# Kernel optimization log

Measured on AMD Instinct MI355X. Metric: run time of the kernel, lower is better.

The kernel has to match this reference:

```python
import jax, jax.numpy as jnp
import numpy as np
from jax import lax

HEADS, DIM_HEAD, KSZ = 8, 64, 3


def conv1x1(x, w):
    # x: [B, Cin, X, Y], w: [Cout, Cin]
    return jnp.einsum('oi,bixy->boxy', w, x)


def setup_inputs() -> dict:
    key = jax.random.key(0)
    ks = jax.random.split(key, 8)
    dim = 256
    inner = HEADS * DIM_HEAD  # 512
    B, H, W = 4, 64, 64
    s = 0.02
    return {
        'fmap': jax.random.normal(ks[0], (B, dim, H, W), jnp.float32),
        'w_lin_q': jax.random.normal(ks[1], (inner, dim), jnp.float32) * s,
        'w_lin_kv_dw': jax.random.normal(ks[2], (dim, 1, 3, 3), jnp.float32) * s,
        'w_lin_kv_pw': jax.random.normal(ks[3], (2 * inner, dim), jnp.float32) * s,
        'w_q': jax.random.normal(ks[4], (inner, dim), jnp.float32) * s,
        'w_kv': jax.random.normal(ks[5], (2 * inner, dim), jnp.float32) * s,
        'w_out': jax.random.normal(ks[6], (dim, 2 * inner), jnp.float32) * s,
        'b_out': jax.random.normal(ks[7], (dim,), jnp.float32) * s,
    }


def reference(fmap, w_lin_q, w_lin_kv_dw, w_lin_kv_pw, w_q, w_kv, w_out, b_out):
    B, dim, X, Y = fmap.shape
    h, d, ksz = HEADS, DIM_HEAD, KSZ
    scale = d ** -0.5
    n = X * Y

    # ---- linear (global) attention branch ----
    # depthwise 3x3 conv (groups=dim) then pointwise 1x1, both bias-free
    dw = lax.conv_general_dilated(
        fmap, w_lin_kv_dw, window_strides=(1, 1), padding=[(1, 1), (1, 1)],
        dimension_numbers=('NCHW', 'OIHW', 'NCHW'), feature_group_count=dim)
    lin_kv = conv1x1(dw, w_lin_kv_pw)
    lin_q = conv1x1(fmap, w_lin_q)
    lin_k, lin_v = jnp.split(lin_kv, 2, axis=1)

    def to_bhnd(t):  # [B, h*d, X, Y] -> [B, h, n, d]
        return t.reshape(B, h, d, n).transpose(0, 1, 3, 2)

    lq, lk, lv = to_bhnd(lin_q), to_bhnd(lin_k), to_bhnd(lin_v)
    lq = jax.nn.softmax(lq, axis=-1) * scale   # softmax over feature dim
    lk = jax.nn.softmax(lk, axis=-2)           # softmax over sequence dim
    ctx = jnp.einsum('bhnd,bhne->bhde', lk, lv)
    lin_out = jnp.einsum('bhnd,bhde->bhne', lq, ctx)
    lin_out = lin_out.transpose(0, 1, 3, 2).reshape(B, h * d, X, Y)
    lin_out = jax.nn.gelu(lin_out, approximate=False)  # torch nn.GELU (exact erf)

    # ---- local window attention branch (unfold equivalent) ----
    q = conv1x1(fmap, w_q).reshape(B, h, d, X, Y) * scale
    kv = conv1x1(fmap, w_kv)
    k, v = jnp.split(kv, 2, axis=1)
    k = k.reshape(B, h, d, X, Y)
    v = v.reshape(B, h, d, X, Y)
    pad = ksz // 2
    padw = ((0, 0), (0, 0), (0, 0), (pad, pad), (pad, pad))
    kp = jnp.pad(k, padw)  # zero padding, as in F.unfold
    vp = jnp.pad(v, padw)
    # j enumerates kernel offsets row-major (ky, kx) -> matches F.unfold layout
    k_win = jnp.stack([kp[..., i:i + X, j:j + Y]
                       for i in range(ksz) for j in range(ksz)], axis=2)  # [B,h,j,d,X,Y]
    v_win = jnp.stack([vp[..., i:i + X, j:j + Y]
                       for i in range(ksz) for j in range(ksz)], axis=2)
    sim = jnp.einsum('bhdxy,bhjdxy->bhxyj', q, k_win)
    attn = jax.nn.softmax(sim, axis=-1)  # stable (max-subtracted internally)
    full = jnp.einsum('bhxyj,bhjdxy->bhdxy', attn, v_win)
    full = full.reshape(B, h * d, X, Y)

    out = jnp.concatenate([lin_out, full], axis=1)  # [B, 2*inner, X, Y]
    return conv1x1(out, w_out) + b_out[None, :, None, None]
```

## Files before the change

kernel.cpp:

```cpp
#include <hip/hip_runtime.h>
#include <cmath>

#define NPIX 4096
#define NTOT 16384
#define CIN  256

typedef __bf16 bf16x8 __attribute__((ext_vector_type(8)));
typedef float  f32x4  __attribute__((ext_vector_type(4)));
typedef unsigned short u16x8 __attribute__((ext_vector_type(8)));

static __device__ __forceinline__ unsigned short f2bf(float f) {
    unsigned u = __float_as_uint(f);
    unsigned r = (u + 0x7FFFu + ((u >> 16) & 1u)) >> 16;
    return (unsigned short)r;
}
static __device__ __forceinline__ float bf2f(unsigned short u) {
    return __uint_as_float((unsigned)u << 16);
}

__global__ __launch_bounds__(256) void k_transpose_bf(const float* __restrict__ src,
                                                      unsigned short* __restrict__ dst) {
    __shared__ float tile[64][65];
    int p0 = blockIdx.x * 64;
    int c0 = blockIdx.y * 64;
    int b  = blockIdx.z;
    int t = threadIdx.x;
    int tp = t & 63, tg = t >> 6;
    const float* s = src + ((size_t)(b * 256 + c0) * 4096) + p0;
#pragma unroll
    for (int r = 0; r < 16; ++r) {
        int c = r * 4 + tg;
        tile[tp][c] = s[(size_t)c * 4096 + tp];
    }
    __syncthreads();
    unsigned short* d = dst + ((size_t)(b * 4096 + p0)) * 256 + c0;
#pragma unroll
    for (int r = 0; r < 16; ++r) {
        int pr = r * 4 + tg;
        d[(size_t)pr * 256 + tp] = f2bf(tile[pr][tp]);
    }
}

__global__ __launch_bounds__(256) void k_dwconv_bf(const unsigned short* __restrict__ FMB,
                                                   const float* __restrict__ wdw,
                                                   unsigned short* __restrict__ DWB) {
    __shared__ float wl[2560];
    int t = threadIdx.x;
    for (int i = t; i < 2304; i += 256) wl[(i / 9) * 10 + (i % 9)] = wdw[i];
    __syncthreads();
    int idx = blockIdx.x * 256 + t;
    int cg = idx & 31, p = idx >> 5;
    int xy = p & 4095, x = xy >> 6, y = xy & 63;
    const unsigned short* base = FMB + (size_t)p * 256 + cg * 8;
    float s[8] = {0.f, 0.f, 0.f, 0.f, 0.f, 0.f, 0.f, 0.f};
#pragma unroll
    for (int dx = 0; dx < 3; ++dx) {
        int xx = x + dx - 1;
        if ((unsigned)xx >= 64u) continue;
#pragma unroll
        for (int dy = 0; dy < 3; ++dy) {
            int yy = y + dy - 1;
            if ((unsigned)yy >= 64u) continue;
            u16x8 v = *(const u16x8*)(base + ((dx - 1) * 64 + (dy - 1)) * 256);
#pragma unroll
            for (int d = 0; d < 8; ++d)
                s[d] += bf2f(v[d]) * wl[(cg * 8 + d) * 10 + dx * 3 + dy];
        }
    }
    uint4 w0;
    w0.x = (unsigned)f2bf(s[0]) | ((unsigned)f2bf(s[1]) << 16);
    w0.y = (unsigned)f2bf(s[2]) | ((unsigned)f2bf(s[3]) << 16);
    w0.z = (unsigned)f2bf(s[4]) | ((unsigned)f2bf(s[5]) << 16);
    w0.w = (unsigned)f2bf(s[6]) | ((unsigned)f2bf(s[7]) << 16);
    *(uint4*)(DWB + (size_t)p * 256 + cg * 8) = w0;
}

__global__ __launch_bounds__(256) void k_convert_w(const float* __restrict__ w1, const float* __restrict__ w2,
                                                   const float* __restrict__ w3, const float* __restrict__ w4,
                                                   const float* __restrict__ w5,
                                                   unsigned short* __restrict__ dst) {
    int i = blockIdx.x * 256 + threadIdx.x;
    float v;
    if (i < 131072)       v = w1[i];
    else if (i < 262144)  v = w2[i - 131072];
    else if (i < 524288)  v = w3[i - 262144];
    else if (i < 786432) {
        int elem = i - 524288;
        int rp = elem >> 8, c = elem & 255;
        int h = rp >> 7, wi = rp & 127;
        int srow = (wi < 64) ? (h * 64 + wi) : (512 + h * 64 + (wi - 64));
        v = w4[srow * 256 + c];
    } else                v = w5[i - 786432];
    dst[i] = f2bf(v);
}

__global__ __launch_bounds__(256) void k_g1_gemm(const __bf16* __restrict__ A,
                                                 const __bf16* __restrict__ B,
                                                 unsigned short* __restrict__ LQBT,
                                                 unsigned short* __restrict__ CKV2T) {
    __shared__ __align__(16) __bf16 SMEM[32768];
    const int K = 256;
    const int m0 = blockIdx.x * 128;
    const int n0 = blockIdx.y * 128;
    const int t = threadIdx.x;
    const int w = t >> 6, l = t & 63;
    const int wm = (w >> 1) * 64, wn = (w & 1) * 64;
    f32x4 acc[4][4];
#pragma unroll
    for (int i = 0; i < 4; ++i)
#pragma unroll
        for (int j = 0; j < 4; ++j) acc[i][j] = (f32x4){0.f, 0.f, 0.f, 0.f};

    const int lrow = l >> 3;
    const int lchunk = (l & 7) ^ lrow;
    auto STAGE = [&](int buf, int k0) {
#pragma unroll
        for (int r = 0; r < 4; ++r) {
            const int s = w + r * 4;
            const int row = s * 8 + lrow;
            const __bf16* ga = A + (size_t)(m0 + row) * K + (k0 + lchunk * 8);
            const __bf16* gb = B + (size_t)(n0 + row) * K + (k0 + lchunk * 8);
            __builtin_amdgcn_global_load_lds((const __attribute__((address_space(1))) void*)ga,
                                             (__attribute__((address_space(3))) void*)(SMEM + buf * 16384 + s * 512),
                                             16, 0, 0);
            __builtin_amdgcn_global_load_lds((const __attribute__((address_space(1))) void*)gb,
                                             (__attribute__((address_space(3))) void*)(SMEM + buf * 16384 + 8192 + s * 512),
                                             16, 0, 0);
        }
    };
    STAGE(0, 0);
    STAGE(1, 64);
#pragma unroll
    for (int it = 0; it < 4; ++it) {
        if (it < 3) { asm volatile("s_waitcnt vmcnt(8)" ::: "memory"); }
        else        { asm volatile("s_waitcnt vmcnt(0)" ::: "memory"); }
        __builtin_amdgcn_sched_barrier(0);
        __builtin_amdgcn_s_barrier();
        __builtin_amdgcn_sched_barrier(0);
        const __bf16* As = SMEM + (it & 1) * 16384;
        const __bf16* Bs = As + 8192;
#pragma unroll
        for (int ks = 0; ks < 2; ++ks) {
            bf16x8 af[4], bfr[4];
#pragma unroll
            for (int i = 0; i < 4; ++i) {
                const int arow = wm + i * 16 + (l & 15);
                const int ac = ((l >> 4) + ks * 4) ^ (l & 7);
                af[i] = *(const bf16x8*)(As + arow * 64 + ac * 8);
                const int brow = wn + i * 16 + (l & 15);
                bfr[i] = *(const bf16x8*)(Bs + brow * 64 + ac * 8);
            }
#pragma unroll
            for (int i = 0; i < 4; ++i)
#pragma unroll
                for (int j = 0; j < 4; ++j)
                    acc[i][j] = __builtin_amdgcn_mfma_f32_16x16x32_bf16(af[i], bfr[j], acc[i][j], 0, 0, 0);
        }
        __builtin_amdgcn_sched_barrier(0);
        __builtin_amdgcn_s_barrier();
        __builtin_amdgcn_sched_barrier(0);
        if (it < 2) STAGE(it & 1, (it + 2) * 64);
    }

#pragma unroll
    for (int i = 0; i < 4; ++i) {
        const int prow = wm + i * 16 + (l >> 4) * 4;
#pragma unroll
        for (int j = 0; j < 4; ++j) {
            const int col = wn + j * 16 + (l & 15);
            const int cglob = n0 + col;
            const float sc = (cglob >= 512 && cglob < 1024) ? 0.125f : 1.f;
#pragma unroll
            for (int q = 0; q < 4; ++q)
                *((unsigned short*)SMEM + (prow + q) * 136 + col) = f2bf(acc[i][j][q] * sc);
        }
    }
    __syncthreads();
    const int pix = t >> 1, half = t & 1;
    unsigned short* sp = (unsigned short*)SMEM + pix * 136 + half * 64;
    if (n0 < 512) {
        float m = -1e30f;
#pragma unroll
        for (int r = 0; r < 8; ++r) {
            u16x8 v = *(const u16x8*)(sp + r * 8);
#pragma unroll
            for (int d = 0; d < 8; ++d) m = fmaxf(m, bf2f(v[d]));
        }
        float Z = 0.f;
#pragma unroll
        for (int r = 0; r < 8; ++r) {
            u16x8 v = *(const u16x8*)(sp + r * 8);
            u16x8 e;
#pragma unroll
            for (int d = 0; d < 8; ++d) {
                float ev = __expf(bf2f(v[d]) - m);
                Z += ev;
                e[d] = f2bf(ev);
            }
            *(u16x8*)(sp + r * 8) = e;
        }
        float inv = 0.125f / Z;
        unsigned short* dst = LQBT + ((size_t)(n0 >> 7) << 21) + (size_t)m0 * 128 + t * 64;
#pragma unroll
        for (int r = 0; r < 8; ++r) {
            u16x8 e = *(const u16x8*)(sp + r * 8);
            float o[8];
#pragma unroll
            for (int d = 0; d < 8; ++d) o[d] = bf2f(e[d]) * inv;
            uint4 wv;
            wv.x = (unsigned)f2bf(o[0]) | ((unsigned)f2bf(o[1]) << 16);
            wv.y = (unsigned)f2bf(o[2]) | ((unsigned)f2bf(o[3]) << 16);
            wv.z = (unsigned)f2bf(o[4]) | ((unsigned)f2bf(o[5]) << 16);
            wv.w = (unsigned)f2bf(o[6]) | ((unsigned)f2bf(o[7]) << 16);
            *(uint4*)(dst + r * 8) = wv;
        }
    } else {
        unsigned short* dptr = CKV2T + ((size_t)((n0 - 512) >> 7) << 21) + (size_t)m0 * 128 + t * 64;
#pragma unroll
        for (int r = 0; r < 8; ++r)
            *(u16x8*)(dptr + r * 8) = *(const u16x8*)(sp + r * 8);
    }
}

__global__ __launch_bounds__(256) void k_g2_gemm(const __bf16* __restrict__ A,
                                                 const __bf16* __restrict__ B,
                                                 float* __restrict__ PART,
                                                 float* __restrict__ S) {
    __shared__ __align__(16) __bf16 SMEM[32768];
    const int K = 256;
    const int m0 = blockIdx.x * 128;
    const int n0 = blockIdx.y * 128;
    const int t = threadIdx.x;
    const int w = t >> 6, l = t & 63;
    const int wm = (w >> 1) * 64, wn = (w & 1) * 64;
    f32x4 acc[4][4];
#pragma unroll
    for (int i = 0; i < 4; ++i)
#pragma unroll
        for (int j = 0; j < 4; ++j) acc[i][j] = (f32x4){0.f, 0.f, 0.f, 0.f};

    const int lrow = l >> 3;
    const int lchunk = (l & 7) ^ lrow;
    auto STAGE = [&](int buf, int k0) {
#pragma unroll
        for (int r = 0; r < 4; ++r) {
            const int s = w + r * 4;
            const int row = s * 8 + lrow;
            const __bf16* ga = A + (size_t)(m0 + row) * K + (k0 + lchunk * 8);
            const __bf16* gb = B + (size_t)(n0 + row) * K + (k0 + lchunk * 8);
            __builtin_amdgcn_global_load_lds((const __attribute__((address_space(1))) void*)ga,
                                             (__attribute__((address_space(3))) void*)(SMEM + buf * 16384 + s * 512),
                                             16, 0, 0);
            __builtin_amdgcn_global_load_lds((const __attribute__((address_space(1))) void*)gb,
                                             (__attribute__((address_space(3))) void*)(SMEM + buf * 16384 + 8192 + s * 512),
                                             16, 0, 0);
        }
    };
    STAGE(0, 0);
    STAGE(1, 64);
#pragma unroll
    for (int it = 0; it < 4; ++it) {
        if (it < 3) { asm volatile("s_waitcnt vmcnt(8)" ::: "memory"); }
        else        { asm volatile("s_waitcnt vmcnt(0)" ::: "memory"); }
        __builtin_amdgcn_sched_barrier(0);
        __builtin_amdgcn_s_barrier();
        __builtin_amdgcn_sched_barrier(0);
        const __bf16* As = SMEM + (it & 1) * 16384;
        const __bf16* Bs = As + 8192;
#pragma unroll
        for (int ks = 0; ks < 2; ++ks) {
            bf16x8 af[4], bfr[4];
#pragma unroll
            for (int i = 0; i < 4; ++i) {
                const int arow = wm + i * 16 + (l & 15);
                const int ac = ((l >> 4) + ks * 4) ^ (l & 7);
                af[i] = *(const bf16x8*)(As + arow * 64 + ac * 8);
                const int brow = wn + i * 16 + (l & 15);
                bfr[i] = *(const bf16x8*)(Bs + brow * 64 + ac * 8);
            }
#pragma unroll
            for (int i = 0; i < 4; ++i)
#pragma unroll
                for (int j = 0; j < 4; ++j)
                    acc[i][j] = __builtin_amdgcn_mfma_f32_16x16x32_bf16(af[i], bfr[j], acc[i][j], 0, 0, 0);
        }
        __builtin_amdgcn_sched_barrier(0);
        __builtin_amdgcn_s_barrier();
        __builtin_amdgcn_sched_barrier(0);
        if (it < 2) STAGE(it & 1, (it + 2) * 64);
    }

    unsigned short* ST = (unsigned short*)SMEM;
#pragma unroll
    for (int i = 0; i < 4; ++i) {
        const int prow = wm + i * 16 + (l >> 4) * 4;
#pragma unroll
        for (int j = 0; j < 4; ++j) {
            const int col = wn + j * 16 + (l & 15);
#pragma unroll
            for (int q = 0; q < 4; ++q) {
                float v = acc[i][j][q];
                ST[col * 130 + prow + q] = f2bf(col < 64 ? __expf(v) : v);
            }
        }
    }
    __syncthreads();
    const int h  = blockIdx.y;
    const int bh = (m0 >> 12) * 8 + h;
    const int dm = (w >> 1) * 32, en = (w & 1) * 32;
    f32x4 c2[2][2];
    f32x4 s2[2];
#pragma unroll
    for (int i = 0; i < 2; ++i) {
        s2[i] = (f32x4){0.f, 0.f, 0.f, 0.f};
#pragma unroll
        for (int j = 0; j < 2; ++j) c2[i][j] = (f32x4){0.f, 0.f, 0.f, 0.f};
    }
    bf16x8 ones;
#pragma unroll
    for (int d = 0; d < 8; ++d) ones[d] = (__bf16)1.0f;
#pragma unroll
    for (int kp = 0; kp < 4; ++kp) {
        bf16x8 af2[2], bv2[2];
#pragma unroll
        for (int i = 0; i < 2; ++i) {
            const int drow = dm + i * 16 + (l & 15);
            af2[i] = *(const bf16x8*)(ST + drow * 130 + kp * 32 + (l >> 4) * 8);
            const int erow = 64 + en + i * 16 + (l & 15);
            bv2[i] = *(const bf16x8*)(ST + erow * 130 + kp * 32 + (l >> 4) * 8);
        }
#pragma unroll
        for (int i = 0; i < 2; ++i)
#pragma unroll
            for (int j = 0; j < 2; ++j)
                c2[i][j] = __builtin_amdgcn_mfma_f32_16x16x32_bf16(af2[i], bv2[j], c2[i][j], 0, 0, 0);
        if ((w & 1) == 0)
#pragma unroll
            for (int i = 0; i < 2; ++i)
                s2[i] = __builtin_amdgcn_mfma_f32_16x16x32_bf16(af2[i], ones, s2[i], 0, 0, 0);
    }
    float* pp = PART + ((size_t)((m0 >> 7) * 8 + h)) * 4096 + t * 16;
#pragma unroll
    for (int i = 0; i < 2; ++i)
#pragma unroll
        for (int j = 0; j < 2; ++j)
            *(f32x4*)(pp + (i * 2 + j) * 4) = c2[i][j];
    if ((w & 1) == 0 && (l & 15) == 0) {
#pragma unroll
        for (int i = 0; i < 2; ++i)
#pragma unroll
            for (int q = 0; q < 4; ++q)
                atomicAdd(&S[bh * 64 + dm + i * 16 + (l >> 4) * 4 + q], s2[i][q]);
    }
}

__global__ __launch_bounds__(256) void k_ctxnorm(const float* __restrict__ PART,
                                                 const float* __restrict__ S,
                                                 unsigned short* __restrict__ ctxb) {
    __shared__ float SUM[1024];
    __shared__ float sinv[32];
    const int bh = blockIdx.x, wq = blockIdx.y;
    const int b = bh >> 3, h = bh & 7;
    const int t = threadIdx.x;
    const int bd = (wq >> 1) * 32, be = (wq & 1) * 32;
#pragma unroll
    for (int r = 0; r < 4; ++r) {
        const int kl = t + 256 * r;
        const float* src = PART + (size_t)((b * 32) * 8 + h) * 4096 + wq * 1024 + kl;
        float s = 0.f;
#pragma unroll
        for (int mi = 0; mi < 32; ++mi)
            s += src[(size_t)mi * 8 * 4096];
        SUM[kl] = s;
    }
    if (t < 32) sinv[t] = 1.f / S[bh * 64 + bd + t];
    __syncthreads();
#pragma unroll
    for (int r = 0; r < 4; ++r) {
        const int idx = t + 256 * r;
        const int dd = idx & 31, ee = idx >> 5;
        const int d = bd + dd, e = be + ee;
        const int l2 = (((d >> 2) & 3) << 4) | (e & 15);
        const int i2 = (d >> 4) & 1, j2 = (e >> 4) & 1, q = d & 3;
        const int kl = l2 * 16 + (i2 * 2 + j2) * 4 + q;
        ctxb[(size_t)bh * 4096 + e * 64 + d] = f2bf(SUM[kl] * sinv[dd]);
    }
}

__global__ __launch_bounds__(256) void k_out_gemm(const __bf16* __restrict__ A,
                                                  const __bf16* __restrict__ B,
                                                  float* __restrict__ C,
                                                  const float* __restrict__ bias) {
    __shared__ __align__(16) __bf16 SMEM[24576];
    const int K = 1024;
    const int m0 = blockIdx.x * 64, n0 = blockIdx.y * 128;
    const int t = threadIdx.x;
    const int w = t >> 6, l = t & 63;
    const int wm = (w >> 1) * 32, wn = (w & 1) * 64;
    f32x4 acc[2][4];
#pragma unroll
    for (int i = 0; i < 2; ++i)
#pragma unroll
        for (int j = 0; j < 4; ++j) acc[i][j] = (f32x4){0.f, 0.f, 0.f, 0.f};

    const int lrow = l >> 3;
    const int lchunk = (l & 7) ^ lrow;
    auto STAGE = [&](int buf, int k0) {
        __bf16* As = SMEM + buf * 12288;
        __bf16* Bs = As + 4096;
#pragma unroll
        for (int r = 0; r < 2; ++r) {
            const int s = w + r * 4;
            const int row = s * 8 + lrow;
            const __bf16* ga = A + (size_t)(m0 + row) * K + (k0 + lchunk * 8);
            __builtin_amdgcn_global_load_lds((const __attribute__((address_space(1))) void*)ga,
                                             (__attribute__((address_space(3))) void*)(As + s * 512),
                                             16, 0, 0);
        }
#pragma unroll
        for (int r = 0; r < 4; ++r) {
            const int s = w + r * 4;
            const int row = s * 8 + lrow;
            const __bf16* gb = B + (size_t)(n0 + row) * K + (k0 + lchunk * 8);
            __builtin_amdgcn_global_load_lds((const __attribute__((address_space(1))) void*)gb,
                                             (__attribute__((address_space(3))) void*)(Bs + s * 512),
                                             16, 0, 0);
        }
    };

    STAGE(0, 0);
    STAGE(1, 64);
    for (int it = 0; it < 16; ++it) {
        if (it < 15) { asm volatile("s_waitcnt vmcnt(6)" ::: "memory"); }
        else         { asm volatile("s_waitcnt vmcnt(0)" ::: "memory"); }
        __builtin_amdgcn_sched_barrier(0);
        __builtin_amdgcn_s_barrier();
        __builtin_amdgcn_sched_barrier(0);
        const __bf16* As = SMEM + (it & 1) * 12288;
        const __bf16* Bs = As + 4096;
#pragma unroll
        for (int ks = 0; ks < 2; ++ks) {
            const int ac = ((l >> 4) + ks * 4) ^ (l & 7);
            bf16x8 af[2], bfr[4];
#pragma unroll
            for (int i = 0; i < 2; ++i) {
                const int arow = wm + i * 16 + (l & 15);
                af[i] = *(const bf16x8*)(As + arow * 64 + ac * 8);
            }
#pragma unroll
            for (int j = 0; j < 4; ++j) {
                const int brow = wn + j * 16 + (l & 15);
                bfr[j] = *(const bf16x8*)(Bs + brow * 64 + ac * 8);
            }
#pragma unroll
            for (int i = 0; i < 2; ++i)
#pragma unroll
                for (int j = 0; j < 4; ++j)
                    acc[i][j] = __builtin_amdgcn_mfma_f32_16x16x32_bf16(af[i], bfr[j], acc[i][j], 0, 0, 0);
        }
        __builtin_amdgcn_sched_barrier(0);
        __builtin_amdgcn_s_barrier();
        __builtin_amdgcn_sched_barrier(0);
        if (it < 14) STAGE(it & 1, (it + 2) * 64);
    }
    const int b = m0 >> 12;
#pragma unroll
    for (int j = 0; j < 4; ++j) {
        const int col = n0 + wn + j * 16 + (l & 15);
        const float bv = bias[col];
        float* obase = C + ((size_t)(b * 256 + col) << 12);
#pragma unroll
        for (int i = 0; i < 2; ++i) {
            const int rb = (m0 & 4095) + wm + i * 16 + (l >> 4) * 4;
            f32x4 v = acc[i][j];
            v[0] += bv; v[1] += bv; v[2] += bv; v[3] += bv;
            *(f32x4*)(obase + rb) = v;
        }
    }
}

__global__ __launch_bounds__(256) void k_linlocal(const __bf16* __restrict__ LQBT,
                                                  const __bf16* __restrict__ ctxb,
                                                  const unsigned short* __restrict__ CKV,
                                                  unsigned short* __restrict__ CAT) {
    const int bid = blockIdx.x;
    const int t = threadIdx.x;
    if (bid < 1024) {
        const int p0 = (bid & 127) * 128;
        const int h  = bid >> 7;
        const int b  = p0 >> 12;
        const int w = t >> 6, l = t & 63;
        const int wm = w * 32;
        const __bf16* Bm = ctxb + (size_t)(b * 8 + h) * 4096;
        const __bf16* Ah = LQBT + ((size_t)(h >> 1) << 21) + (h & 1) * 64;
        f32x4 acc[2][4];
#pragma unroll
        for (int i = 0; i < 2; ++i)
#pragma unroll
            for (int j = 0; j < 4; ++j) acc[i][j] = (f32x4){0.f, 0.f, 0.f, 0.f};
#pragma unroll
        for (int ks = 0; ks < 2; ++ks) {
            const int c = (l >> 4) + ks * 4;
            bf16x8 af[2], bfr[4];
#pragma unroll
            for (int i = 0; i < 2; ++i) {
                const int row = p0 + wm + i * 16 + (l & 15);
                af[i] = *(const bf16x8*)(Ah + (size_t)row * 128 + c * 8);
            }
#pragma unroll
            for (int j = 0; j < 4; ++j) {
                const int erow = j * 16 + (l & 15);
                bfr[j] = *(const bf16x8*)(Bm + erow * 64 + c * 8);
            }
#pragma unroll
            for (int i = 0; i < 2; ++i)
#pragma unroll
                for (int j = 0; j < 4; ++j)
                    acc[i][j] = __builtin_amdgcn_mfma_f32_16x16x32_bf16(af[i], bfr[j], acc[i][j], 0, 0, 0);
        }
#pragma unroll
        for (int i = 0; i < 2; ++i) {
#pragma unroll
            for (int j = 0; j < 4; ++j) {
                const int e = j * 16 + (l & 15);
#pragma unroll
                for (int q = 0; q < 4; ++q) {
                    const int p = p0 + wm + i * 16 + (l >> 4) * 4 + q;
                    float x = acc[i][j][q];
                    float g = 0.5f * x * (1.f + erff(x * 0.70710678118654752f));
                    CAT[(size_t)p * 1024 + h * 64 + e] = f2bf(g);
                }
            }
        }
    } else {
        const int W = (bid - 1024) * 4 + (t >> 6);
        const int lane = t & 63;
        const int h = W & 7;
        const int G = W >> 3;
        const int yg = G & 7, x = (G >> 3) & 63, b = G >> 9;
        const int lg = lane >> 3, c8 = lane & 7;
        const int y = (yg << 3) + lg;
        const int p = (b << 12) + (x << 6) + y;
        const unsigned short* Qp = CKV + ((size_t)(h >> 1) << 21) + (size_t)p * 128 + (h & 1) * 64 + c8 * 8;
        const unsigned short* Kp = Qp + ((size_t)4 << 21);
        const unsigned short* Vp = Qp + ((size_t)8 << 21);

        const bool okx[3] = {x > 0, true, x < 63};
        const bool oky[3] = {y > 0, true, y < 63};
        bool okn[9]; int ofs[9];
#pragma unroll
        for (int dx = 0; dx < 3; ++dx)
#pragma unroll
            for (int dy = 0; dy < 3; ++dy) {
                const int k = dx * 3 + dy;
                okn[k] = okx[dx] && oky[dy];
                ofs[k] = okn[k] ? ((dx - 1) * 64 + (dy - 1)) * 128 : 0;
            }
        float qf[8];
        {
            u16x8 q8 = *(const u16x8*)Qp;
#pragma unroll
            for (int d = 0; d < 8; ++d) qf[d] = bf2f(q8[d]);
        }
        float sim[9];
#pragma unroll
        for (int k = 0; k < 9; ++k) {
            u16x8 k8 = *(const u16x8*)(Kp + ofs[k]);
            float s = 0.f;
#pragma unroll
            for (int d = 0; d < 8; ++d) s += qf[d] * bf2f(k8[d]);
            s = okn[k] ? s : 0.f;
            s += __shfl_xor(s, 1);
            s += __shfl_xor(s, 2);
            s += __shfl_xor(s, 4);
            sim[k] = s;
        }
        float mx = sim[0];
#pragma unroll
        for (int k = 1; k < 9; ++k) mx = fmaxf(mx, sim[k]);
        float a[9], Z = 0.f;
#pragma unroll
        for (int k = 0; k < 9; ++k) { a[k] = __expf(sim[k] - mx); Z += a[k]; }
        float inv = 1.f / Z;
#pragma unroll
        for (int k = 0; k < 9; ++k) a[k] = okn[k] ? a[k] * inv : 0.f;
        float o[8] = {0.f, 0.f, 0.f, 0.f, 0.f, 0.f, 0.f, 0.f};
#pragma unroll
        for (int k = 0; k < 9; ++k) {
            u16x8 v8 = *(const u16x8*)(Vp + ofs[k]);
#pragma unroll
            for (int d = 0; d < 8; ++d) o[d] += a[k] * bf2f(v8[d]);
        }
        unsigned short* dst = CAT + (size_t)p * 1024 + 512 + h * 64 + c8 * 8;
        uint4 w0;
        w0.x = (unsigned)f2bf(o[0]) | ((unsigned)f2bf(o[1]) << 16);
        w0.y = (unsigned)f2bf(o[2]) | ((unsigned)f2bf(o[3]) << 16);
        w0.z = (unsigned)f2bf(o[4]) | ((unsigned)f2bf(o[5]) << 16);
        w0.w = (unsigned)f2bf(o[6]) | ((unsigned)f2bf(o[7]) << 16);
        *(uint4*)dst = w0;
    }
}

extern "C" void kernel_launch(void* const* d_in, const int* in_sizes, int n_in,
                              void* d_out, int out_size, void* d_ws, size_t ws_size,
                              hipStream_t stream) {
    const float* fmap  = (const float*)d_in[0];
    const float* w_lq  = (const float*)d_in[1];
    const float* w_dw  = (const float*)d_in[2];
    const float* w_pw  = (const float*)d_in[3];
    const float* w_q   = (const float*)d_in[4];
    const float* w_kv  = (const float*)d_in[5];
    const float* w_out = (const float*)d_in[6];
    const float* b_out = (const float*)d_in[7];
    float* out = (float*)d_out;

    unsigned short* base = (unsigned short*)d_ws;
    unsigned short* CATB = base;
    unsigned short* FMB  = base + (size_t)NTOT * 1024;
    unsigned short* DWB  = FMB + (size_t)NTOT * 256;
    unsigned short* WB   = DWB + (size_t)NTOT * 256;
    unsigned short* WQKV = WB;
    unsigned short* WPW  = WB + 524288;
    unsigned short* WOUT = WB + 786432;
    unsigned short* CTXB = WB + 1048576;
    unsigned short* LQBT = CTXB + 131072;
    unsigned short* CKV2T= LQBT + (size_t)NTOT * 512;
    float* PART = (float*)(CKV2T + (size_t)NTOT * 1536);
    float* S    = PART + (size_t)1024 * 4096;

    k_transpose_bf<<<dim3(64, 4, 4), 256, 0, stream>>>(fmap, FMB);
    k_convert_w<<<4096, 256, 0, stream>>>(w_lq, w_q, w_kv, w_pw, w_out, WB);
    hipMemsetAsync(S, 0, 2048 * sizeof(float), stream);
    k_dwconv_bf<<<2048, 256, 0, stream>>>(FMB, w_dw, DWB);
    k_g2_gemm<<<dim3(128, 8), 256, 0, stream>>>((const __bf16*)DWB, (const __bf16*)WPW, PART, S);
    k_g1_gemm<<<dim3(128, 16), 256, 0, stream>>>((const __bf16*)FMB, (const __bf16*)WQKV, LQBT, CKV2T);
    k_ctxnorm<<<dim3(32, 4), 256, 0, stream>>>(PART, S, CTXB);
    k_linlocal<<<5120, 256, 0, stream>>>((const __bf16*)LQBT, (const __bf16*)CTXB, CKV2T, CATB);
    k_out_gemm<<<dim3(256, 2), 256, 0, stream>>>((const __bf16*)CATB, (const __bf16*)WOUT, out, b_out);
}
```

Measured before the change: 168.1 us.

## Fuse linear-attention q·ctx matmul and GELU into the QKV GEMM epilogue

The lin-q softmax epilogue of the first GEMM now keeps the normalized queries in shared memory and multiplies them directly by the per-head context matrix with MFMA, applying GELU and writing into the concat buffer. The LQBT intermediate buffer and its global write/read round trip go away, and the k_linlocal kernel shrinks to local attention only. The context normalization kernel is moved ahead of the QKV GEMM so the context is ready, which serializes that dependency and adds extra work and a barrier to the GEMM epilogue.

```diff
diff --git a/kernel.cpp b/kernel.cpp
--- a/kernel.cpp
+++ b/kernel.cpp
@@ -96,8 +96,9 @@
 
 __global__ __launch_bounds__(256) void k_g1_gemm(const __bf16* __restrict__ A,
                                                  const __bf16* __restrict__ B,
-                                                 unsigned short* __restrict__ LQBT,
-                                                 unsigned short* __restrict__ CKV2T) {
+                                                 const __bf16* __restrict__ ctxb,
+                                                 unsigned short* __restrict__ CKV2T,
+                                                 unsigned short* __restrict__ CAT) {
     __shared__ __align__(16) __bf16 SMEM[32768];
     const int K = 256;
     const int m0 = blockIdx.x * 128;
@@ -162,6 +163,7 @@
         if (it < 2) STAGE(it & 1, (it + 2) * 64);
     }
 
+    unsigned short* SU = (unsigned short*)SMEM;
 #pragma unroll
     for (int i = 0; i < 4; ++i) {
         const int prow = wm + i * 16 + (l >> 4) * 4;
@@ -172,13 +174,13 @@
             const float sc = (cglob >= 512 && cglob < 1024) ? 0.125f : 1.f;
 #pragma unroll
             for (int q = 0; q < 4; ++q)
-                *((unsigned short*)SMEM + (prow + q) * 136 + col) = f2bf(acc[i][j][q] * sc);
+                SU[(prow + q) * 136 + col] = f2bf(acc[i][j][q] * sc);
         }
     }
     __syncthreads();
-    const int pix = t >> 1, half = t & 1;
-    unsigned short* sp = (unsigned short*)SMEM + pix * 136 + half * 64;
     if (n0 < 512) {
+        const int pix = t >> 1, half = t & 1;
+        unsigned short* sp = SU + pix * 136 + half * 64;
         float m = -1e30f;
 #pragma unroll
         for (int r = 0; r < 8; ++r) {
@@ -200,21 +202,61 @@
             *(u16x8*)(sp + r * 8) = e;
         }
         float inv = 0.125f / Z;
-        unsigned short* dst = LQBT + ((size_t)(n0 >> 7) << 21) + (size_t)m0 * 128 + t * 64;
 #pragma unroll
         for (int r = 0; r < 8; ++r) {
             u16x8 e = *(const u16x8*)(sp + r * 8);
-            float o[8];
-#pragma unroll
-            for (int d = 0; d < 8; ++d) o[d] = bf2f(e[d]) * inv;
-            uint4 wv;
-            wv.x = (unsigned)f2bf(o[0]) | ((unsigned)f2bf(o[1]) << 16);
-            wv.y = (unsigned)f2bf(o[2]) | ((unsigned)f2bf(o[3]) << 16);
-            wv.z = (unsigned)f2bf(o[4]) | ((unsigned)f2bf(o[5]) << 16);
-            wv.w = (unsigned)f2bf(o[6]) | ((unsigned)f2bf(o[7]) << 16);
-            *(uint4*)(dst + r * 8) = wv;
+#pragma unroll
+            for (int d = 0; d < 8; ++d) e[d] = f2bf(bf2f(e[d]) * inv);
+            *(u16x8*)(sp + r * 8) = e;
+        }
+        __syncthreads();
+        const int h2 = w >> 1;
+        const int h  = (n0 >> 6) + h2;
+        const int rb = (w & 1) * 64;
+        const int bimg = m0 >> 12;
+        const __bf16* Bm = ctxb + (size_t)(bimg * 8 + h) * 4096;
+        f32x4 a2[4][4];
+#pragma unroll
+        for (int i = 0; i < 4; ++i)
+#pragma unroll
+            for (int j = 0; j < 4; ++j) a2[i][j] = (f32x4){0.f, 0.f, 0.f, 0.f};
+#pragma unroll
+        for (int ks = 0; ks < 2; ++ks) {
+            const int c = (l >> 4) + ks * 4;
+            bf16x8 af[4], bfr[4];
+#pragma unroll
+            for (int i = 0; i < 4; ++i) {
+                const int arow = rb + i * 16 + (l & 15);
+                af[i] = *(const bf16x8*)((const __bf16*)SU + arow * 136 + h2 * 64 + c * 8);
+            }
+#pragma unroll
+            for (int j = 0; j < 4; ++j) {
+                const int erow = j * 16 + (l & 15);
+                bfr[j] = *(const bf16x8*)(Bm + erow * 64 + c * 8);
+            }
+#pragma unroll
+            for (int i = 0; i < 4; ++i)
+#pragma unroll
+                for (int j = 0; j < 4; ++j)
+                    a2[i][j] = __builtin_amdgcn_mfma_f32_16x16x32_bf16(af[i], bfr[j], a2[i][j], 0, 0, 0);
+        }
+#pragma unroll
+        for (int i = 0; i < 4; ++i) {
+#pragma unroll
+            for (int j = 0; j < 4; ++j) {
+                const int e = j * 16 + (l & 15);
+#pragma unroll
+                for (int q = 0; q < 4; ++q) {
+                    const int p = m0 + rb + i * 16 + (l >> 4) * 4 + q;
+                    float x = a2[i][j][q];
+                    float g = 0.5f * x * (1.f + erff(x * 0.70710678118654752f));
+                    CAT[(size_t)p * 1024 + h * 64 + e] = f2bf(g);
+                }
+            }
         }
     } else {
+        const int pix = t >> 1, half = t & 1;
+        const unsigned short* sp = SU + pix * 136 + half * 64;
         unsigned short* dptr = CKV2T + ((size_t)((n0 - 512) >> 7) << 21) + (size_t)m0 * 128 + t * 64;
 #pragma unroll
         for (int r = 0; r < 8; ++r)
@@ -479,126 +521,73 @@
     }
 }
 
-__global__ __launch_bounds__(256) void k_linlocal(const __bf16* __restrict__ LQBT,
-                                                  const __bf16* __restrict__ ctxb,
-                                                  const unsigned short* __restrict__ CKV,
-                                                  unsigned short* __restrict__ CAT) {
-    const int bid = blockIdx.x;
-    const int t = threadIdx.x;
-    if (bid < 1024) {
-        const int p0 = (bid & 127) * 128;
-        const int h  = bid >> 7;
-        const int b  = p0 >> 12;
-        const int w = t >> 6, l = t & 63;
-        const int wm = w * 32;
-        const __bf16* Bm = ctxb + (size_t)(b * 8 + h) * 4096;
-        const __bf16* Ah = LQBT + ((size_t)(h >> 1) << 21) + (h & 1) * 64;
-        f32x4 acc[2][4];
-#pragma unroll
-        for (int i = 0; i < 2; ++i)
-#pragma unroll
-            for (int j = 0; j < 4; ++j) acc[i][j] = (f32x4){0.f, 0.f, 0.f, 0.f};
-#pragma unroll
-        for (int ks = 0; ks < 2; ++ks) {
-            const int c = (l >> 4) + ks * 4;
-            bf16x8 af[2], bfr[4];
-#pragma unroll
-            for (int i = 0; i < 2; ++i) {
-                const int row = p0 + wm + i * 16 + (l & 15);
-                af[i] = *(const bf16x8*)(Ah + (size_t)row * 128 + c * 8);
-            }
-#pragma unroll
-            for (int j = 0; j < 4; ++j) {
-                const int erow = j * 16 + (l & 15);
-                bfr[j] = *(const bf16x8*)(Bm + erow * 64 + c * 8);
-            }
-#pragma unroll
-            for (int i = 0; i < 2; ++i)
-#pragma unroll
-                for (int j = 0; j < 4; ++j)
-                    acc[i][j] = __builtin_amdgcn_mfma_f32_16x16x32_bf16(af[i], bfr[j], acc[i][j], 0, 0, 0);
-        }
-#pragma unroll
-        for (int i = 0; i < 2; ++i) {
-#pragma unroll
-            for (int j = 0; j < 4; ++j) {
-                const int e = j * 16 + (l & 15);
-#pragma unroll
-                for (int q = 0; q < 4; ++q) {
-                    const int p = p0 + wm + i * 16 + (l >> 4) * 4 + q;
-                    float x = acc[i][j][q];
-                    float g = 0.5f * x * (1.f + erff(x * 0.70710678118654752f));
-                    CAT[(size_t)p * 1024 + h * 64 + e] = f2bf(g);
-                }
-            }
-        }
-    } else {
-        const int W = (bid - 1024) * 4 + (t >> 6);
-        const int lane = t & 63;
-        const int h = W & 7;
-        const int G = W >> 3;
-        const int yg = G & 7, x = (G >> 3) & 63, b = G >> 9;
-        const int lg = lane >> 3, c8 = lane & 7;
-        const int y = (yg << 3) + lg;
-        const int p = (b << 12) + (x << 6) + y;
-        const unsigned short* Qp = CKV + ((size_t)(h >> 1) << 21) + (size_t)p * 128 + (h & 1) * 64 + c8 * 8;
-        const unsigned short* Kp = Qp + ((size_t)4 << 21);
-        const unsigned short* Vp = Qp + ((size_t)8 << 21);
-
-        const bool okx[3] = {x > 0, true, x < 63};
-        const bool oky[3] = {y > 0, true, y < 63};
-        bool okn[9]; int ofs[9];
-#pragma unroll
-        for (int dx = 0; dx < 3; ++dx)
-#pragma unroll
-            for (int dy = 0; dy < 3; ++dy) {
-                const int k = dx * 3 + dy;
-                okn[k] = okx[dx] && oky[dy];
-                ofs[k] = okn[k] ? ((dx - 1) * 64 + (dy - 1)) * 128 : 0;
-            }
-        float qf[8];
-        {
-            u16x8 q8 = *(const u16x8*)Qp;
-#pragma unroll
-            for (int d = 0; d < 8; ++d) qf[d] = bf2f(q8[d]);
-        }
-        float sim[9];
-#pragma unroll
-        for (int k = 0; k < 9; ++k) {
-            u16x8 k8 = *(const u16x8*)(Kp + ofs[k]);
-            float s = 0.f;
-#pragma unroll
-            for (int d = 0; d < 8; ++d) s += qf[d] * bf2f(k8[d]);
-            s = okn[k] ? s : 0.f;
-            s += __shfl_xor(s, 1);
-            s += __shfl_xor(s, 2);
-            s += __shfl_xor(s, 4);
-            sim[k] = s;
-        }
-        float mx = sim[0];
-#pragma unroll
-        for (int k = 1; k < 9; ++k) mx = fmaxf(mx, sim[k]);
-        float a[9], Z = 0.f;
-#pragma unroll
-        for (int k = 0; k < 9; ++k) { a[k] = __expf(sim[k] - mx); Z += a[k]; }
-        float inv = 1.f / Z;
-#pragma unroll
-        for (int k = 0; k < 9; ++k) a[k] = okn[k] ? a[k] * inv : 0.f;
-        float o[8] = {0.f, 0.f, 0.f, 0.f, 0.f, 0.f, 0.f, 0.f};
-#pragma unroll
-        for (int k = 0; k < 9; ++k) {
-            u16x8 v8 = *(const u16x8*)(Vp + ofs[k]);
-#pragma unroll
-            for (int d = 0; d < 8; ++d) o[d] += a[k] * bf2f(v8[d]);
-        }
-        unsigned short* dst = CAT + (size_t)p * 1024 + 512 + h * 64 + c8 * 8;
-        uint4 w0;
-        w0.x = (unsigned)f2bf(o[0]) | ((unsigned)f2bf(o[1]) << 16);
-        w0.y = (unsigned)f2bf(o[2]) | ((unsigned)f2bf(o[3]) << 16);
-        w0.z = (unsigned)f2bf(o[4]) | ((unsigned)f2bf(o[5]) << 16);
-        w0.w = (unsigned)f2bf(o[6]) | ((unsigned)f2bf(o[7]) << 16);
-        *(uint4*)dst = w0;
-    }
+__global__ __launch_bounds__(256) void k_local_attn(const unsigned short* __restrict__ CKV,
+                                                    unsigned short* __restrict__ CAT) {
+    const int W = blockIdx.x * 4 + (threadIdx.x >> 6);
+    const int lane = threadIdx.x & 63;
+    const int h = W & 7;
+    const int G = W >> 3;
+    const int yg = G & 7, x = (G >> 3) & 63, b = G >> 9;
+    const int lg = lane >> 3, c8 = lane & 7;
+    const int y = (yg << 3) + lg;
+    const int p = (b << 12) + (x << 6) + y;
+    const unsigned short* Qp = CKV + ((size_t)(h >> 1) << 21) + (size_t)p * 128 + (h & 1) * 64 + c8 * 8;
+    const unsigned short* Kp = Qp + ((size_t)4 << 21);
+    const unsigned short* Vp = Qp + ((size_t)8 << 21);
+
+    const bool okx[3] = {x > 0, true, x < 63};
+    const bool oky[3] = {y > 0, true, y < 63};
+    bool okn[9]; int ofs[9];
+#pragma unroll
+    for (int dx = 0; dx < 3; ++dx)
+#pragma unroll
+        for (int dy = 0; dy < 3; ++dy) {
+            const int k = dx * 3 + dy;
+            okn[k] = okx[dx] && oky[dy];
+            ofs[k] = okn[k] ? ((dx - 1) * 64 + (dy - 1)) * 128 : 0;
+        }
+    float qf[8];
+    {
+        u16x8 q8 = *(const u16x8*)Qp;
+#pragma unroll
+        for (int d = 0; d < 8; ++d) qf[d] = bf2f(q8[d]);
+    }
+    float sim[9];
+#pragma unroll
+    for (int k = 0; k < 9; ++k) {
+        u16x8 k8 = *(const u16x8*)(Kp + ofs[k]);
+        float s = 0.f;
+#pragma unroll
+        for (int d = 0; d < 8; ++d) s += qf[d] * bf2f(k8[d]);
+        s = okn[k] ? s : 0.f;
+        s += __shfl_xor(s, 1);
+        s += __shfl_xor(s, 2);
+        s += __shfl_xor(s, 4);
+        sim[k] = s;
+    }
+    float mx = sim[0];
+#pragma unroll
+    for (int k = 1; k < 9; ++k) mx = fmaxf(mx, sim[k]);
+    float a[9], Z = 0.f;
+#pragma unroll
+    for (int k = 0; k < 9; ++k) { a[k] = __expf(sim[k] - mx); Z += a[k]; }
+    float inv = 1.f / Z;
+#pragma unroll
+    for (int k = 0; k < 9; ++k) a[k] = okn[k] ? a[k] * inv : 0.f;
+    float o[8] = {0.f, 0.f, 0.f, 0.f, 0.f, 0.f, 0.f, 0.f};
+#pragma unroll
+    for (int k = 0; k < 9; ++k) {
+        u16x8 v8 = *(const u16x8*)(Vp + ofs[k]);
+#pragma unroll
+        for (int d = 0; d < 8; ++d) o[d] += a[k] * bf2f(v8[d]);
+    }
+    unsigned short* dst = CAT + (size_t)p * 1024 + 512 + h * 64 + c8 * 8;
+    uint4 w0;
+    w0.x = (unsigned)f2bf(o[0]) | ((unsigned)f2bf(o[1]) << 16);
+    w0.y = (unsigned)f2bf(o[2]) | ((unsigned)f2bf(o[3]) << 16);
+    w0.z = (unsigned)f2bf(o[4]) | ((unsigned)f2bf(o[5]) << 16);
+    w0.w = (unsigned)f2bf(o[6]) | ((unsigned)f2bf(o[7]) << 16);
+    *(uint4*)dst = w0;
 }
 
 extern "C" void kernel_launch(void* const* d_in, const int* in_sizes, int n_in,
@@ -623,8 +612,7 @@
     unsigned short* WPW  = WB + 524288;
     unsigned short* WOUT = WB + 786432;
     unsigned short* CTXB = WB + 1048576;
-    unsigned short* LQBT = CTXB + 131072;
-    unsigned short* CKV2T= LQBT + (size_t)NTOT * 512;
+    unsigned short* CKV2T= CTXB + 131072;
     float* PART = (float*)(CKV2T + (size_t)NTOT * 1536);
     float* S    = PART + (size_t)1024 * 4096;
 
@@ -633,8 +621,9 @@
     hipMemsetAsync(S, 0, 2048 * sizeof(float), stream);
     k_dwconv_bf<<<2048, 256, 0, stream>>>(FMB, w_dw, DWB);
     k_g2_gemm<<<dim3(128, 8), 256, 0, stream>>>((const __bf16*)DWB, (const __bf16*)WPW, PART, S);
-    k_g1_gemm<<<dim3(128, 16), 256, 0, stream>>>((const __bf16*)FMB, (const __bf16*)WQKV, LQBT, CKV2T);
     k_ctxnorm<<<dim3(32, 4), 256, 0, stream>>>(PART, S, CTXB);
-    k_linlocal<<<5120, 256, 0, stream>>>((const __bf16*)LQBT, (const __bf16*)CTXB, CKV2T, CATB);
+    k_g1_gemm<<<dim3(128, 16), 256, 0, stream>>>((const __bf16*)FMB, (const __bf16*)WQKV,
+                                                 (const __bf16*)CTXB, CKV2T, CATB);
+    k_local_attn<<<4096, 256, 0, stream>>>(CKV2T, CATB);
     k_out_gemm<<<dim3(256, 2), 256, 0, stream>>>((const __bf16*)CATB, (const __bf16*)WOUT, out, b_out);
 }
```

Result: no change. 165.8 us (-1.4%).
